# Kernel optimization log

Measured on AMD Instinct MI355X. Metric: run time of the kernel, lower is better.

## Reference

```python
import math
import jax, jax.numpy as jnp
import numpy as np

B, P, L = 32, 128, 64
DIN, TE, H, NH, NL = 16, 64, 512, 8, 2
DH = H // NH
DP = DIN + TE
TAU = 300.0
DELTA = 300.0

_PARAM_SPEC = [
    ("te_scale_w", (1, 1)), ("te_scale_b", (1,)),
    ("te_per_w", (TE - 1, 1)), ("te_per_b", (TE - 1,)),
    ("inp_w", (H, DP)), ("inp_b", (H,)),
    ("wq", (H, H)), ("bq", (H,)), ("wk", (H, H)), ("bk", (H,)),
    ("wv", (H, H)), ("bv", (H,)), ("wo", (H, H)), ("bo", (H,)),
    ("ffn_w1", (H, H)), ("ffn_b1", (H,)), ("ffn_w2", (H, H)), ("ffn_b2", (H,)),
    ("ln1_g", (H,)), ("ln1_b", (H,)), ("ln2_g", (H,)), ("ln2_b", (H,)),
    ("exists_bias", (1, 1, H)),
    ("gwq", (NL, H, H)), ("gbq", (NL, H)), ("gwk", (NL, H, H)), ("gbk", (NL, H)),
    ("gwv", (NL, H, H)), ("gbv", (NL, H)), ("gwo", (NL, H, H)), ("gbo", (NL, H)),
]


def setup_inputs() -> dict:
    key = jax.random.key(0)
    ks = jax.random.split(key, 3 + len(_PARAM_SPEC))
    inp = {
        "x": jax.random.normal(ks[0], (B, P, L, DIN), jnp.float32),
        "tt": jax.random.uniform(ks[1], (B, P, L, 1), jnp.float32),
        "mask": jax.random.randint(ks[2], (B, P, L, 1), 0, 2).astype(jnp.int32),
    }
    for i, (name, shp) in enumerate(_PARAM_SPEC):
        inp[name] = 0.02 * jax.random.normal(ks[3 + i], shp, jnp.float32)
    # LayerNorm affine params: gamma=1, beta=0
    inp["ln1_g"] = jnp.ones((H,), jnp.float32)
    inp["ln1_b"] = jnp.zeros((H,), jnp.float32)
    inp["ln2_g"] = jnp.ones((H,), jnp.float32)
    inp["ln2_b"] = jnp.zeros((H,), jnp.float32)
    return inp


def _layernorm(x, g, b, eps=1e-5):
    m = x.mean(-1, keepdims=True)
    v = ((x - m) ** 2).mean(-1, keepdims=True)
    return (x - m) / jnp.sqrt(v + eps) * g + b


def _time_bias(m):
    idx = jnp.arange(m)
    dist = jnp.abs(idx[:, None] - idx[None, :]).astype(jnp.float32) * DELTA
    return jnp.log(jnp.exp(-dist / TAU) + 1e-12)  # [P, P]


def _pos_encoding(p, d):
    pos = jnp.arange(p, dtype=jnp.float32)[:, None]
    div = jnp.exp(jnp.arange(0, d, 2, dtype=jnp.float32) * (-math.log(10000.0) / d))
    pe = jnp.zeros((p, d), jnp.float32)
    pe = pe.at[:, 0::2].set(jnp.sin(pos * div))
    pe = pe.at[:, 1::2].set(jnp.cos(pos * div))
    return pe


def reference(x, tt, mask,
              te_scale_w, te_scale_b, te_per_w, te_per_b,
              inp_w, inp_b, wq, bq, wk, bk, wv, bv, wo, bo,
              ffn_w1, ffn_b1, ffn_w2, ffn_b2, ln1_g, ln1_b, ln2_g, ln2_b,
              exists_bias, gwq, gbq, gwk, gbk, gwv, gbv, gwo, gbo):
    b, p, l, _ = x.shape
    # --- Learnable time embedding: scale linear + sin(periodic linear), concat ---
    te1 = tt @ te_scale_w.T + te_scale_b                      # [B,P,L,1]
    te2 = jnp.sin(tt @ te_per_w.T + te_per_b)                 # [B,P,L,TE-1]
    pts = jnp.concatenate([x, te1, te2], axis=-1)             # [B,P,L,DP]

    valid = (mask[..., 0] > 0).reshape(b * p, l)              # [N,L] bool
    h = (pts.reshape(b * p, l, DP) @ inp_w.T) + inp_b         # [N,L,H]

    has_any = jnp.any(valid, axis=1)                          # [N]
    key_pad = ~valid
    # Empty patches: unmask position 0 and zero its features
    key_pad = key_pad.at[:, 0].set(key_pad[:, 0] & has_any)
    pos0 = (jnp.arange(l) == 0)[None, :, None]
    h = jnp.where((~has_any)[:, None, None] & pos0, 0.0, h)

    # --- Intra-patch MHA (GAT) ---
    def heads(t, w, bias):
        return ((t @ w.T) + bias).reshape(b * p, l, NH, DH)
    q, k, v = heads(h, wq, bq), heads(h, wk, bk), heads(h, wv, bv)
    sc = jnp.einsum("nqhd,nkhd->nhqk", q, k) / math.sqrt(DH)
    sc = jnp.where(key_pad[:, None, None, :], -1e9, sc)
    z = jnp.einsum("nhqk,nkhd->nqhd", jax.nn.softmax(sc, axis=-1), v)
    z = z.reshape(b * p, l, H) @ wo.T + bo
    h = _layernorm(h + z, ln1_g, ln1_b)
    ffn = jax.nn.relu(h @ ffn_w1.T + ffn_b1) @ ffn_w2.T + ffn_b2
    h = _layernorm(h + ffn, ln2_g, ln2_b)

    # Masked mean pooling -> patch tokens
    w = valid.astype(jnp.float32)[..., None]                  # [N,L,1]
    denom = jnp.clip(w.sum(axis=1), 1.0)
    h = ((h * w).sum(axis=1) / denom).reshape(b, p, H)        # [B,P,H]

    # Exists bias for missing patches + positional encoding
    pexists = has_any.reshape(b, p).astype(jnp.float32)       # [B,P]
    h = h + exists_bias * (1.0 - pexists)[..., None]
    h = h + _pos_encoding(p, H)[None]

    # --- Patch-level time-biased graph attention stack (residual) ---
    tb = _time_bias(p)[None, None]                            # [1,1,P,P]
    kp = (pexists <= 0.0)[:, None, None, :]                   # [B,1,1,P]
    for li in range(NL):
        def gh(t, w, bias):
            return ((t @ w.T) + bias).reshape(b, p, NH, DH)
        q = gh(h, gwq[li], gbq[li])
        k = gh(h, gwk[li], gbk[li])
        v = gh(h, gwv[li], gbv[li])
        att = jnp.einsum("bqhd,bkhd->bhqk", q, k) / math.sqrt(DH) + tb
        att = jnp.where(kp, -1e9, att)
        out = jnp.einsum("bhqk,bkhd->bqhd", jax.nn.softmax(att, axis=-1), v)
        out = out.reshape(b, p, H) @ gwo[li].T + gbo[li]
        out = out * pexists[..., None]
        h = h + out
    return h
```

## Files before the change

kernel.cpp:

```cpp
#include <hip/hip_runtime.h>

#define NTOK 4096
#define CH   512
#define NCHUNK 8

typedef _Float16 f16;
typedef __attribute__((ext_vector_type(8))) _Float16 half8;
typedef __attribute__((ext_vector_type(4))) _Float16 half4;
typedef __attribute__((ext_vector_type(4))) float f32x4;

#define OFF_INPW 0
#define OFF_WQKV (512*128)
#define OFF_WO   (OFF_WQKV + 3*512*512)
#define OFF_W1   (OFF_WO + 512*512)
#define OFF_W2   (OFF_W1 + 512*512)
#define OFF_GW   (OFF_W2 + 512*512)
#define WBF_TOT  (OFF_GW + 8*512*512)

static __device__ __forceinline__ f32x4 mfma16(half8 a, half8 b, f32x4 c){
  return __builtin_amdgcn_mfma_f32_16x16x32_f16(a, b, c, 0, 0, 0);
}

static __device__ __forceinline__ void gld_lds16(const f16* g, f16* l){
  __builtin_amdgcn_global_load_lds(
      (const __attribute__((address_space(1))) void*)g,
      (__attribute__((address_space(3))) void*)l, 16, 0, 0);
}

#define FULL_BARRIER() do { \
    asm volatile("" ::: "memory"); \
    __builtin_amdgcn_s_barrier(); \
    __builtin_amdgcn_sched_barrier(0); \
  } while(0)

__global__ __launch_bounds__(256) void conv_weights(
    const float* __restrict__ inpw, const float* __restrict__ wq, const float* __restrict__ wk,
    const float* __restrict__ wv, const float* __restrict__ wo, const float* __restrict__ w1,
    const float* __restrict__ w2, const float* __restrict__ gwq, const float* __restrict__ gwk,
    const float* __restrict__ gwv, const float* __restrict__ gwo, f16* __restrict__ wbf,
    const float* __restrict__ bq, const float* __restrict__ bk, const float* __restrict__ bv,
    const float* __restrict__ gbq, const float* __restrict__ gbk, const float* __restrict__ gbv,
    float* __restrict__ biasb)
{
  int e = blockIdx.x*256 + threadIdx.x;
  int y = blockIdx.y;
  if (y == 0){
    if (e < 512*128){
      int row = e>>7, col = e&127;
      float v = (col < 80) ? inpw[row*80 + col] : 0.f;
      wbf[OFF_INPW + e] = (f16)v;
    }
    return;
  }
  if (y == 15){
    if (e < 1536){
      biasb[e] = (e < 512) ? bq[e] : (e < 1024 ? bk[e-512] : bv[e-1024]);
    } else if (e < 3*1536){
      int idx = e - 1536, li = idx/1536, c = idx - li*1536;
      float v = (c < 512) ? gbq[li*512 + c] : (c < 1024 ? gbk[li*512 + c-512] : gbv[li*512 + c-1024]);
      biasb[e] = v;
    }
    return;
  }
  if (e >= 512*512) return;
  const float* src; int off;
  if (y <= 6){
    const float* tab[6] = {wq, wk, wv, wo, w1, w2};
    src = tab[y-1]; off = OFF_WQKV + (y-1)*512*512;
  } else {
    int idx = y-7; int li = idx>>2, part = idx&3;
    const float* tab[4] = {gwq, gwk, gwv, gwo};
    src = tab[part] + (size_t)li*512*512; off = OFF_GW + idx*512*512;
  }
  wbf[off + e] = (f16)src[e];
}

__global__ __launch_bounds__(256) void build_mask(
    const int* __restrict__ mask, float* __restrict__ mb, float* __restrict__ pex)
{
  int wv = threadIdx.x>>6, lane = threadIdx.x&63;
  int n = blockIdx.x*4 + wv;
  int valid = mask[(size_t)n*64 + lane] > 0;
  unsigned long long ball = __ballot(valid);
  int hasany = (ball != 0ull);
  int masked = (lane == 0) ? (!valid && hasany) : (!valid);
  mb[(size_t)n*64 + lane] = masked ? -1e9f : 0.f;
  if (lane == 0) pex[n] = hasany ? 1.f : 0.f;
}

__global__ __launch_bounds__(256) void pts_build(
    const float* __restrict__ x, const float* __restrict__ tt,
    const float* __restrict__ tsw, const float* __restrict__ tsb,
    const float* __restrict__ tpw, const float* __restrict__ tpb,
    f16* __restrict__ pts, int rowbase)
{
  int e = blockIdx.x*256 + threadIdx.x;
  int r = e>>7, col = e&127;
  size_t grow = (size_t)rowbase + r;
  float v;
  if (col < 16) v = x[grow*16 + col];
  else if (col >= 80) v = 0.f;
  else {
    float t = tt[grow];
    if (col == 16) v = t*tsw[0] + tsb[0];
    else           v = __sinf(t*tpw[col-17] + tpb[col-17]);
  }
  pts[e] = (f16)v;
}

template<int RESID, bool RELU, bool OUTF32, bool ZEMPTY>
__global__ __launch_bounds__(256) void gemm128(
    const f16* __restrict__ A, const f16* __restrict__ W, const float* __restrict__ bias,
    void* __restrict__ Cout, const void* __restrict__ Rsd, const float* __restrict__ pex,
    int K, int lda, int ldc, int nbase, f16* __restrict__ dual)
{
  __shared__ __align__(16) f16 As[128][64];
  __shared__ __align__(16) f16 Bs[128][64];
  const int tid = threadIdx.x;
  const int m0 = blockIdx.x*128, n0 = blockIdx.y*128;
  const int wv = tid>>6, lane = tid&63, l15 = lane&15, quad = lane>>4;
  const int wm = (wv&1)*64, wn = (wv>>1)*64;
  const int srow = lane>>3;
  const int schunk = (lane&7) ^ srow;
  f32x4 acc[4][4] = {};
  for (int kc = 0; kc < K; kc += 64){
    __syncthreads();
    #pragma unroll
    for (int i=0; i<4; i++){
      const int rA = wv*32 + i*8;
      gld_lds16(A + (size_t)(m0 + rA + srow)*lda + kc + schunk*8, &As[rA][0]);
      gld_lds16(W + (size_t)(n0 + rA + srow)*K   + kc + schunk*8, &Bs[rA][0]);
    }
    __syncthreads();
    #pragma unroll
    for (int kk=0; kk<2; kk++){
      half8 av[4], bv8[4];
      #pragma unroll
      for (int t=0; t<4; t++){
        const int ra = wm + t*16 + l15;
        av[t]  = *(const half8*)(&As[ra][(((kk*4 + quad) ^ (ra&7)))*8]);
        const int rb = wn + t*16 + l15;
        bv8[t] = *(const half8*)(&Bs[rb][(((kk*4 + quad) ^ (rb&7)))*8]);
      }
      #pragma unroll
      for (int mt=0; mt<4; mt++)
        #pragma unroll
        for (int nt=0; nt<4; nt++)
          acc[mt][nt] = mfma16(av[mt], bv8[nt], acc[mt][nt]);
    }
  }
  #pragma unroll
  for (int mt=0; mt<4; mt++){
    #pragma unroll
    for (int nt=0; nt<4; nt++){
      #pragma unroll
      for (int i=0; i<4; i++){
        int gr = m0 + wm + mt*16 + quad*4 + i;
        int gc = n0 + wn + nt*16 + l15;
        float v = acc[mt][nt][i] + bias[gc];
        if (RELU) v = fmaxf(v, 0.f);
        if (RESID == 1) v += (float)((const f16*)Rsd)[(size_t)gr*ldc + gc];
        if (ZEMPTY){ if ((gr&63)==0 && pex[nbase + (gr>>6)]==0.f) v = 0.f; }
        if (RESID == 2) v = v*pex[gr] + ((const float*)Rsd)[(size_t)gr*ldc + gc];
        if (OUTF32) ((float*)Cout)[(size_t)gr*ldc + gc] = v;
        else        ((f16*)Cout)[(size_t)gr*ldc + gc] = (f16)v;
        if (RESID == 2){ if (dual) dual[(size_t)gr*ldc + gc] = (f16)v; }
      }
    }
  }
}

template<int RESID, bool RELU>
__global__ __launch_bounds__(512,2) void gemm256(
    const f16* __restrict__ A, const f16* __restrict__ W, const float* __restrict__ bias,
    f16* __restrict__ Cout, const f16* __restrict__ Rsd,
    int K, int lda, int ldc)
{
  __shared__ __align__(16) f16 As[2*2*128*64];
  __shared__ __align__(16) f16 Bs[2*2*128*64];

  const int tid = threadIdx.x;
  const int wv = tid>>6, lane = tid&63, l15 = lane&15, quad = lane>>4;
  const int wm = wv>>2;
  const int wn = wv&3;

  const int gx = gridDim.x, gy = gridDim.y;
  int nwg = gx*gy;
  int orig = blockIdx.x*gy + blockIdx.y;
  int qq = nwg>>3;
  int swz = (orig&7)*qq + (orig>>3);
  const int m0 = (swz/gy)*256, n0 = (swz%gy)*256;

  const int NT = K>>6;

  auto stage_half = [&](int t, int hf){
    int tc = t < NT ? t : NT-1;
    int kc = tc<<6;
    int b  = t & 1;
    #pragma unroll
    for (int i=0;i<2;i++){
      int idx = wv*2+i;
      int row = idx*8 + (lane>>3);
      int col = kc + (((lane&7) ^ (lane>>3))<<3);
      if (hf < 2)
        gld_lds16(A + (size_t)(m0 + hf*128 + row)*lda + col,
                  As + b*16384 + hf*8192 + idx*512);
      else
        gld_lds16(W + (size_t)(n0 + (hf-2)*128 + row)*K + col,
                  Bs + b*16384 + (hf-2)*8192 + idx*512);
    }
  };
  auto ldsA = [&](int b, int mt, int kk)->half8{
    int r = mt*16 + l15;
    int g = kk*4 + quad;
    return *(const half8*)(As + b*16384 + wm*8192 + r*64 + ((g ^ (r&7))<<3));
  };
  auto ldsB = [&](int b, int nt, int kk)->half8{
    int r = (wn&1)*64 + nt*16 + l15;
    int g = kk*4 + quad;
    return *(const half8*)(Bs + b*16384 + (wn>>1)*8192 + r*64 + ((g ^ (r&7))<<3));
  };

  half8 a[8], b0[4], b1[4];
  f32x4 acc[8][4] = {};
  auto mm8 = [&](int mb, half8* bq, int nb){
    __builtin_amdgcn_s_setprio(1);
    #pragma unroll
    for (int m=0;m<4;m++)
      #pragma unroll
      for (int n=0;n<2;n++)
        #pragma unroll
        for (int k=0;k<2;k++)
          acc[mb+m][nb+n] = mfma16(a[m*2+k], bq[n*2+k], acc[mb+m][nb+n]);
    __builtin_amdgcn_s_setprio(0);
  };

  stage_half(0,0); stage_half(0,1); stage_half(0,2); stage_half(0,3);
  stage_half(1,2); stage_half(1,3);
  asm volatile("s_waitcnt vmcnt(4)" ::: "memory");
  FULL_BARRIER();

  for (int t = 0; t < NT; t += 2){
    #pragma unroll
    for (int hv = 0; hv < 2; hv++){
      const int c  = t + hv;
      const int bf = hv;
      #pragma unroll
      for (int m=0;m<4;m++){ a[m*2]=ldsA(bf,m,0); a[m*2+1]=ldsA(bf,m,1); }
      #pragma unroll
      for (int n=0;n<2;n++){ b0[n*2]=ldsB(bf,n,0); b0[n*2+1]=ldsB(bf,n,1); }
      stage_half(c+1, 0);
      FULL_BARRIER();
      mm8(0, b0, 0);
      FULL_BARRIER();
      #pragma unroll
      for (int n=0;n<2;n++){ b1[n*2]=ldsB(bf,n+2,0); b1[n*2+1]=ldsB(bf,n+2,1); }
      stage_half(c+1, 1);
      FULL_BARRIER();
      mm8(0, b1, 2);
      FULL_BARRIER();
      #pragma unroll
      for (int m=0;m<4;m++){ a[m*2]=ldsA(bf,m+4,0); a[m*2+1]=ldsA(bf,m+4,1); }
      stage_half(c+2, 2);
      FULL_BARRIER();
      mm8(4, b1, 2);
      FULL_BARRIER();
      stage_half(c+2, 3);
      asm volatile("s_waitcnt vmcnt(4)" ::: "memory");
      FULL_BARRIER();
      mm8(4, b0, 0);
      FULL_BARRIER();
    }
  }

  #pragma unroll
  for (int mt=0; mt<8; mt++){
    #pragma unroll
    for (int nt=0; nt<4; nt++){
      #pragma unroll
      for (int i=0; i<4; i++){
        int gr = m0 + wm*128 + mt*16 + quad*4 + i;
        int gc = n0 + wn*64  + nt*16 + l15;
        float v = acc[mt][nt][i] + bias[gc];
        if (RELU) v = fmaxf(v, 0.f);
        if (RESID == 1) v += (float)Rsd[(size_t)gr*ldc + gc];
        __builtin_nontemporal_store((f16)v, &Cout[(size_t)gr*ldc + gc]);
      }
    }
  }
}

__global__ __launch_bounds__(128) void attn_patch(
    f16* __restrict__ qkv, const float* __restrict__ maskbias, int nbase)
{
  __shared__ f16 Vt[2][64][72];
  __shared__ f16 Ps[2][64][72];
  __shared__ float mbs[64];
  const int tid = threadIdx.x, wv = tid>>6, lane = tid&63, l15 = lane&15, quad = lane>>4;
  const int n = blockIdx.x, h = blockIdx.y*2 + wv;
  if (tid < 64) mbs[tid] = maskbias[(size_t)(nbase+n)*64 + tid];
  const f16* Vb = qkv + 1024 + h*64;
  for (int i=0; i<64; i++)
    Vt[wv][lane][i] = Vb[((size_t)n*64 + i)*1536 + lane];
  __syncthreads();
  const f16* Qb  = qkv + (size_t)n*64*1536 + h*64;
  const f16* Kbb = Qb + 512;
  f32x4 sacc[4][4] = {};
  #pragma unroll
  for (int kc=0; kc<2; kc++){
    half8 af[4], bf[4];
    #pragma unroll
    for (int t4=0; t4<4; t4++){
      af[t4] = *(const half8*)(Qb  + (size_t)(t4*16 + l15)*1536 + kc*32 + quad*8);
      bf[t4] = *(const half8*)(Kbb + (size_t)(t4*16 + l15)*1536 + kc*32 + quad*8);
    }
    #pragma unroll
    for (int ti=0; ti<4; ti++)
      #pragma unroll
      for (int tj=0; tj<4; tj++)
        sacc[ti][tj] = mfma16(af[ti], bf[tj], sacc[ti][tj]);
  }
  #pragma unroll
  for (int ti=0; ti<4; ti++){
    #pragma unroll
    for (int i=0; i<4; i++){
      float mx = -1e30f;
      #pragma unroll
      for (int tj=0; tj<4; tj++){
        float sv = sacc[ti][tj][i]*0.125f + mbs[tj*16 + l15];
        sacc[ti][tj][i] = sv;
        mx = fmaxf(mx, sv);
      }
      #pragma unroll
      for (int off=1; off<16; off<<=1) mx = fmaxf(mx, __shfl_xor(mx, off, 64));
      float sum = 0.f;
      #pragma unroll
      for (int tj=0; tj<4; tj++){
        float pv = __expf(sacc[ti][tj][i] - mx);
        sacc[ti][tj][i] = pv; sum += pv;
      }
      #pragma unroll
      for (int off=1; off<16; off<<=1) sum += __shfl_xor(sum, off, 64);
      float inv = 1.f/sum;
      int q = ti*16 + quad*4 + i;
      #pragma unroll
      for (int tj=0; tj<4; tj++)
        Ps[wv][q][tj*16 + l15] = (f16)(sacc[ti][tj][i]*inv);
    }
  }
  __syncthreads();
  f32x4 zacc[4][4] = {};
  #pragma unroll
  for (int kc=0; kc<2; kc++){
    half8 va[4], pb[4];
    #pragma unroll
    for (int t4=0; t4<4; t4++){
      va[t4] = *(const half8*)(&Vt[wv][t4*16 + l15][kc*32 + quad*8]);
      pb[t4] = *(const half8*)(&Ps[wv][t4*16 + l15][kc*32 + quad*8]);
    }
    #pragma unroll
    for (int ti2=0; ti2<4; ti2++)
      #pragma unroll
      for (int tj=0; tj<4; tj++)
        zacc[ti2][tj] = mfma16(va[ti2], pb[tj], zacc[ti2][tj]);
  }
  __syncthreads();
  #pragma unroll
  for (int ti2=0; ti2<4; ti2++)
    #pragma unroll
    for (int tj=0; tj<4; tj++){
      int q = tj*16 + l15, d0 = ti2*16 + quad*4;
      half4 pk;
      #pragma unroll
      for (int i=0; i<4; i++) pk[i] = (f16)zacc[ti2][tj][i];
      *(half4*)(&Vt[wv][q][d0]) = pk;
    }
  __syncthreads();
  #pragma unroll
  for (int i=0; i<8; i++){
    int q = i*8 + (lane>>3), d0 = (lane&7)*8;
    *(uint4*)(qkv + ((size_t)n*64 + q)*1536 + h*64 + d0) = *(const uint4*)(&Vt[wv][q][d0]);
  }
}

__global__ __launch_bounds__(256) void ln_rows(
    const f16* __restrict__ X, f16* __restrict__ Y,
    const float* __restrict__ g, const float* __restrict__ b)
{
  int wv = threadIdx.x>>6, lane = threadIdx.x&63;
  size_t row = (size_t)blockIdx.x*4 + wv;
  half8 raw = *(const half8*)(X + row*512 + lane*8);
  float xv[8];
  #pragma unroll
  for (int j=0; j<8; j++) xv[j] = (float)raw[j];
  float s = 0.f;
  #pragma unroll
  for (int j=0; j<8; j++) s += xv[j];
  #pragma unroll
  for (int off=1; off<64; off<<=1) s += __shfl_xor(s, off, 64);
  float mean = s*(1.f/512.f);
  float vs = 0.f;
  #pragma unroll
  for (int j=0; j<8; j++){ float d = xv[j]-mean; vs += d*d; }
  #pragma unroll
  for (int off=1; off<64; off<<=1) vs += __shfl_xor(vs, off, 64);
  float rstd = rsqrtf(vs*(1.f/512.f) + 1e-5f);
  half8 o;
  #pragma unroll
  for (int j=0; j<8; j++){
    int c = lane*8 + j;
    o[j] = (f16)((xv[j]-mean)*rstd*g[c] + b[c]);
  }
  *(half8*)(Y + row*512 + lane*8) = o;
}

__global__ __launch_bounds__(256) void pool_ln2(
    const f16* __restrict__ X, const int* __restrict__ mask,
    const float* __restrict__ g, const float* __restrict__ b, const float* __restrict__ eb,
    float* __restrict__ out, f16* __restrict__ hcopy, int nbase)
{
  __shared__ float mArr[64], rArr[64], vArr[64];
  const int tid = threadIdx.x, wv = tid>>6, lane = tid&63;
  const int n = blockIdx.x, ng = nbase + n, p = ng & 127;
  for (int j=0; j<16; j++){
    int l = wv*16 + j;
    half8 raw = *(const half8*)(X + ((size_t)n*64 + l)*512 + lane*8);
    float s=0.f, ss=0.f;
    #pragma unroll
    for (int jj=0; jj<8; jj++){ float f = (float)raw[jj]; s += f; ss += f*f; }
    #pragma unroll
    for (int off=1; off<64; off<<=1){ s += __shfl_xor(s, off, 64); ss += __shfl_xor(ss, off, 64); }
    if (lane == 0){
      float m = s*(1.f/512.f);
      mArr[l] = m; rArr[l] = rsqrtf(ss*(1.f/512.f) - m*m + 1e-5f);
    }
  }
  if (tid < 64) vArr[tid] = (mask[(size_t)ng*64 + tid] > 0) ? 1.f : 0.f;
  __syncthreads();
  float cnt = 0.f;
  #pragma unroll
  for (int l=0; l<64; l++) cnt += vArr[l];
  float denom = fmaxf(cnt, 1.f);
  float pexv = cnt > 0.f ? 1.f : 0.f;
  float a0=0.f, a1=0.f;
  for (int l=0; l<64; l++){
    float wgt = vArr[l], m = mArr[l], rs = rArr[l];
    float x0 = (float)X[((size_t)n*64+l)*512 + tid];
    float x1 = (float)X[((size_t)n*64+l)*512 + tid + 256];
    a0 += wgt*(x0-m)*rs; a1 += wgt*(x1-m)*rs;
  }
  #pragma unroll
  for (int k=0; k<2; k++){
    int c = tid + k*256;
    float acc = k ? a1 : a0;
    float fr = __expf(-(float)(c & ~1) * (9.210340371976184f/512.f));
    float ang = (float)p * fr;
    float pe = (c & 1) ? cosf(ang) : sinf(ang);
    float o = (g[c]*acc + b[c]*cnt)/denom + eb[c]*(1.f - pexv) + pe;
    out[(size_t)ng*512 + c] = o;
    hcopy[(size_t)ng*512 + c] = (f16)o;
  }
}

__global__ __launch_bounds__(256) void attn_graph(
    f16* __restrict__ qkv, const float* __restrict__ pexists)
{
  __shared__ f16 Vt[64][136];
  __shared__ f16 Ps[4][32][136];
  __shared__ float pxs[128];
  const int tid = threadIdx.x, wv = tid>>6, lane = tid&63, l15 = lane&15, quad = lane>>4;
  const int b = blockIdx.x, h = blockIdx.y;
  if (tid < 128) pxs[tid] = pexists[b*128 + tid];
  const f16* Vb = qkv + 1024 + h*64;
  for (int i=0; i<32; i++){
    int e = tid + i*256, k = e>>6, d = e&63;
    Vt[d][k] = Vb[((size_t)b*128 + k)*1536 + d];
  }
  __syncthreads();
  const f16* Qb = qkv + h*64;
  const f16* Kb = qkv + 512 + h*64;
  const int qb = wv*32;
  f32x4 sacc[2][8] = {};
  #pragma unroll
  for (int kc=0; kc<2; kc++){
    half8 af[2], bf[8];
    #pragma unroll
    for (int ti=0; ti<2; ti++)
      af[ti] = *(const half8*)(Qb + ((size_t)b*128 + qb + ti*16 + l15)*1536 + kc*32 + quad*8);
    #pragma unroll
    for (int tj=0; tj<8; tj++)
      bf[tj] = *(const half8*)(Kb + ((size_t)b*128 + tj*16 + l15)*1536 + kc*32 + quad*8);
    #pragma unroll
    for (int ti=0; ti<2; ti++)
      #pragma unroll
      for (int tj=0; tj<8; tj++)
        sacc[ti][tj] = mfma16(af[ti], bf[tj], sacc[ti][tj]);
  }
  #pragma unroll
  for (int ti=0; ti<2; ti++){
    #pragma unroll
    for (int i=0; i<4; i++){
      int q = qb + ti*16 + quad*4 + i;
      float mx = -1e30f;
      #pragma unroll
      for (int tj=0; tj<8; tj++){
        int col = tj*16 + l15;
        int dd = q - col; if (dd < 0) dd = -dd;
        float tb = __logf(__expf(-(float)dd) + 1e-12f);
        float sv = sacc[ti][tj][i]*0.125f + tb + (pxs[col] > 0.f ? 0.f : -1e9f);
        sacc[ti][tj][i] = sv;
        mx = fmaxf(mx, sv);
      }
      #pragma unroll
      for (int off=1; off<16; off<<=1) mx = fmaxf(mx, __shfl_xor(mx, off, 64));
      float sum = 0.f;
      #pragma unroll
      for (int tj=0; tj<8; tj++){
        float pv = __expf(sacc[ti][tj][i] - mx);
        sacc[ti][tj][i] = pv; sum += pv;
      }
      #pragma unroll
      for (int off=1; off<16; off<<=1) sum += __shfl_xor(sum, off, 64);
      float inv = 1.f/sum;
      int ql = ti*16 + quad*4 + i;
      #pragma unroll
      for (int tj=0; tj<8; tj++)
        Ps[wv][ql][tj*16 + l15] = (f16)(sacc[ti][tj][i]*inv);
    }
  }
  __syncthreads();
  f32x4 zacc[4][2] = {};
  #pragma unroll
  for (int kc=0; kc<4; kc++){
    half8 va[4], pb[2];
    #pragma unroll
    for (int ti2=0; ti2<4; ti2++)
      va[ti2] = *(const half8*)(&Vt[ti2*16 + l15][kc*32 + quad*8]);
    #pragma unroll
    for (int tjq=0; tjq<2; tjq++)
      pb[tjq] = *(const half8*)(&Ps[wv][tjq*16 + l15][kc*32 + quad*8]);
    #pragma unroll
    for (int ti2=0; ti2<4; ti2++)
      #pragma unroll
      for (int tjq=0; tjq<2; tjq++)
        zacc[ti2][tjq] = mfma16(va[ti2], pb[tjq], zacc[ti2][tjq]);
  }
  __syncthreads();
  #pragma unroll
  for (int ti2=0; ti2<4; ti2++)
    #pragma unroll
    for (int tjq=0; tjq<2; tjq++){
      int ql = tjq*16 + l15, d0 = ti2*16 + quad*4;
      half4 pk;
      #pragma unroll
      for (int i=0; i<4; i++) pk[i] = (f16)zacc[ti2][tjq][i];
      *(half4*)(&Ps[wv][ql][d0]) = pk;
    }
  __syncthreads();
  {
    int q = tid>>1, hf = tid&1;
    const f16* src = &Ps[q>>5][q&31][hf*32];
    #pragma unroll
    for (int j=0; j<4; j++)
      *(uint4*)(qkv + ((size_t)b*128 + q)*1536 + h*64 + hf*32 + j*8) = *(const uint4*)(src + j*8);
  }
}

extern "C" void kernel_launch(void* const* d_in, const int* in_sizes, int n_in,
                              void* d_out, int out_size, void* d_ws, size_t ws_size,
                              hipStream_t stream)
{
  (void)in_sizes; (void)n_in; (void)out_size; (void)ws_size;
  const float* x    = (const float*)d_in[0];
  const float* tt   = (const float*)d_in[1];
  const int*   mask = (const int*)  d_in[2];
  const float* tsw  = (const float*)d_in[3];
  const float* tsb  = (const float*)d_in[4];
  const float* tpw  = (const float*)d_in[5];
  const float* tpb  = (const float*)d_in[6];
  const float* inpw = (const float*)d_in[7];
  const float* inpb = (const float*)d_in[8];
  const float* wq   = (const float*)d_in[9];
  const float* bq   = (const float*)d_in[10];
  const float* wk   = (const float*)d_in[11];
  const float* bk   = (const float*)d_in[12];
  const float* wv   = (const float*)d_in[13];
  const float* bv   = (const float*)d_in[14];
  const float* wo   = (const float*)d_in[15];
  const float* bo   = (const float*)d_in[16];
  const float* w1   = (const float*)d_in[17];
  const float* b1   = (const float*)d_in[18];
  const float* w2   = (const float*)d_in[19];
  const float* b2   = (const float*)d_in[20];
  const float* ln1g = (const float*)d_in[21];
  const float* ln1b = (const float*)d_in[22];
  const float* ln2g = (const float*)d_in[23];
  const float* ln2b = (const float*)d_in[24];
  const float* eb   = (const float*)d_in[25];
  const float* gwq  = (const float*)d_in[26];
  const float* gbq  = (const float*)d_in[27];
  const float* gwk  = (const float*)d_in[28];
  const float* gbk  = (const float*)d_in[29];
  const float* gwv  = (const float*)d_in[30];
  const float* gbv  = (const float*)d_in[31];
  const float* gwo  = (const float*)d_in[32];
  const float* gbo  = (const float*)d_in[33];
  float* out = (float*)d_out;

  char* wp = (char*)d_ws;
  auto alloc = [&](size_t bytes)->char*{
    char* p = wp; wp += (bytes + 255) & ~(size_t)255; return p;
  };
  f16*   wbf   = (f16*)  alloc((size_t)WBF_TOT*2);
  float* mb    = (float*)alloc((size_t)NTOK*64*4);
  float* pex   = (float*)alloc((size_t)NTOK*4);
  float* biasb = (float*)alloc((size_t)3*1536*4);
  f16*   ptsb  = (f16*)  alloc((size_t)CH*64*128*2);
  f16*   bufA  = (f16*)  alloc((size_t)CH*64*512*2);
  f16*   bufB  = (f16*)  alloc((size_t)CH*64*512*2);
  f16*   bufC  = (f16*)  alloc((size_t)CH*64*512*2);
  f16*   qkv   = (f16*)  alloc((size_t)CH*64*1536*2);
  f16*   hbf   = (f16*)  alloc((size_t)NTOK*512*2);

  conv_weights<<<dim3(1024,16),256,0,stream>>>(inpw,wq,wk,wv,wo,w1,w2,gwq,gwk,gwv,gwo,wbf,
                                               bq,bk,bv,gbq,gbk,gbv,biasb);
  build_mask<<<NTOK/4,256,0,stream>>>(mask, mb, pex);

  const int MB  = CH*64/128;
  const int MB2 = CH*64/256;
  for (int ch=0; ch<NCHUNK; ch++){
    int nbase = ch*CH;
    int rowbase = nbase*64;
    pts_build<<<CH*64*128/256,256,0,stream>>>(x,tt,tsw,tsb,tpw,tpb,ptsb,rowbase);
    gemm128<0,false,false,true ><<<dim3(MB,4),256,0,stream>>>(ptsb, wbf+OFF_INPW, inpb, bufA, nullptr, pex, 128, 128, 512, nbase, nullptr);
    gemm256<0,false><<<dim3(MB2,6),512,0,stream>>>(bufA, wbf+OFF_WQKV, biasb, qkv, nullptr, 512, 512, 1536);
    attn_patch<<<dim3(CH,4),128,0,stream>>>(qkv, mb, nbase);
    gemm256<1,false><<<dim3(MB2,2),512,0,stream>>>(qkv, wbf+OFF_WO, bo, bufA, bufA, 512, 1536, 512);
    ln_rows<<<CH*64/4,256,0,stream>>>(bufA, bufB, ln1g, ln1b);
    gemm256<0,true ><<<dim3(MB2,2),512,0,stream>>>(bufB, wbf+OFF_W1, b1, bufC, nullptr, 512, 512, 512);
    gemm256<1,false><<<dim3(MB2,2),512,0,stream>>>(bufC, wbf+OFF_W2, b2, bufB, bufB, 512, 512, 512);
    pool_ln2<<<CH,256,0,stream>>>(bufB, mask, ln2g, ln2b, eb, out, hbf, nbase);
  }

  f16* qkvg = bufB;
  for (int li=0; li<2; li++){
    gemm128<0,false,false,false><<<dim3(32,12),256,0,stream>>>(hbf, wbf+OFF_GW + (size_t)li*4*512*512, biasb + 1536*(1+li), qkvg, nullptr, nullptr, 512, 512, 1536, 0, nullptr);
    attn_graph<<<dim3(32,8),256,0,stream>>>(qkvg, pex);
    gemm128<2,false,true ,false><<<dim3(32,4),256,0,stream>>>(qkvg, wbf+OFF_GW + (size_t)(li*4+3)*512*512, gbo+li*512, out, out, pex, 512, 1536, 512, 0, (li==0)? hbf : nullptr);
  }
}
```

Before: 2.614 ms.

## Triple-buffer A tiles with prefetch distance two in gemm256 main loop

```diff
diff --git a/kernel.cpp b/kernel.cpp
--- a/kernel.cpp
+++ b/kernel.cpp
@@ -176,7 +176,7 @@
     f16* __restrict__ Cout, const f16* __restrict__ Rsd,
     int K, int lda, int ldc)
 {
-  __shared__ __align__(16) f16 As[2*2*128*64];
+  __shared__ __align__(16) f16 As[3*2*128*64];
   __shared__ __align__(16) f16 Bs[2*2*128*64];
 
   const int tid = threadIdx.x;
@@ -184,8 +184,8 @@
   const int wm = wv>>2;
   const int wn = wv&3;
 
-  const int gx = gridDim.x, gy = gridDim.y;
-  int nwg = gx*gy;
+  const int gy = gridDim.y;
+  int nwg = gridDim.x*gy;
   int orig = blockIdx.x*gy + blockIdx.y;
   int qq = nwg>>3;
   int swz = (orig&7)*qq + (orig>>3);
@@ -193,32 +193,40 @@
 
   const int NT = K>>6;
 
-  auto stage_half = [&](int t, int hf){
+  auto stageA = [&](int t, int slot, int hf){
     int tc = t < NT ? t : NT-1;
     int kc = tc<<6;
-    int b  = t & 1;
     #pragma unroll
     for (int i=0;i<2;i++){
       int idx = wv*2+i;
       int row = idx*8 + (lane>>3);
       int col = kc + (((lane&7) ^ (lane>>3))<<3);
-      if (hf < 2)
-        gld_lds16(A + (size_t)(m0 + hf*128 + row)*lda + col,
-                  As + b*16384 + hf*8192 + idx*512);
-      else
-        gld_lds16(W + (size_t)(n0 + (hf-2)*128 + row)*K + col,
-                  Bs + b*16384 + (hf-2)*8192 + idx*512);
+      gld_lds16(A + (size_t)(m0 + hf*128 + row)*lda + col,
+                As + slot*16384 + hf*8192 + idx*512);
     }
   };
-  auto ldsA = [&](int b, int mt, int kk)->half8{
+  auto stageB = [&](int t, int hf){
+    int tc = t < NT ? t : NT-1;
+    int kc = tc<<6;
+    int slot = t & 1;
+    #pragma unroll
+    for (int i=0;i<2;i++){
+      int idx = wv*2+i;
+      int row = idx*8 + (lane>>3);
+      int col = kc + (((lane&7) ^ (lane>>3))<<3);
+      gld_lds16(W + (size_t)(n0 + hf*128 + row)*K + col,
+                Bs + slot*16384 + hf*8192 + idx*512);
+    }
+  };
+  auto ldsA = [&](int slot, int mt, int kk)->half8{
     int r = mt*16 + l15;
     int g = kk*4 + quad;
-    return *(const half8*)(As + b*16384 + wm*8192 + r*64 + ((g ^ (r&7))<<3));
+    return *(const half8*)(As + slot*16384 + wm*8192 + r*64 + ((g ^ (r&7))<<3));
   };
-  auto ldsB = [&](int b, int nt, int kk)->half8{
+  auto ldsB = [&](int slot, int nt, int kk)->half8{
     int r = (wn&1)*64 + nt*16 + l15;
     int g = kk*4 + quad;
-    return *(const half8*)(Bs + b*16384 + (wn>>1)*8192 + r*64 + ((g ^ (r&7))<<3));
+    return *(const half8*)(Bs + slot*16384 + (wn>>1)*8192 + r*64 + ((g ^ (r&7))<<3));
   };
 
   half8 a[8], b0[4], b1[4];
@@ -235,42 +243,42 @@
     __builtin_amdgcn_s_setprio(0);
   };
 
-  stage_half(0,0); stage_half(0,1); stage_half(0,2); stage_half(0,3);
-  stage_half(1,2); stage_half(1,3);
-  asm volatile("s_waitcnt vmcnt(4)" ::: "memory");
+  stageA(0,0,0); stageA(0,0,1); stageB(0,0); stageB(0,1);
+  stageA(1,1,0); stageA(1,1,1); stageB(1,0); stageB(1,1);
+  asm volatile("s_waitcnt vmcnt(8)" ::: "memory");
   FULL_BARRIER();
 
-  for (int t = 0; t < NT; t += 2){
-    #pragma unroll
-    for (int hv = 0; hv < 2; hv++){
-      const int c  = t + hv;
-      const int bf = hv;
-      #pragma unroll
-      for (int m=0;m<4;m++){ a[m*2]=ldsA(bf,m,0); a[m*2+1]=ldsA(bf,m,1); }
-      #pragma unroll
-      for (int n=0;n<2;n++){ b0[n*2]=ldsB(bf,n,0); b0[n*2+1]=ldsB(bf,n,1); }
-      stage_half(c+1, 0);
-      FULL_BARRIER();
-      mm8(0, b0, 0);
-      FULL_BARRIER();
-      #pragma unroll
-      for (int n=0;n<2;n++){ b1[n*2]=ldsB(bf,n+2,0); b1[n*2+1]=ldsB(bf,n+2,1); }
-      stage_half(c+1, 1);
-      FULL_BARRIER();
-      mm8(0, b1, 2);
-      FULL_BARRIER();
-      #pragma unroll
-      for (int m=0;m<4;m++){ a[m*2]=ldsA(bf,m+4,0); a[m*2+1]=ldsA(bf,m+4,1); }
-      stage_half(c+2, 2);
-      FULL_BARRIER();
-      mm8(4, b1, 2);
-      FULL_BARRIER();
-      stage_half(c+2, 3);
-      asm volatile("s_waitcnt vmcnt(4)" ::: "memory");
-      FULL_BARRIER();
-      mm8(4, b0, 0);
-      FULL_BARRIER();
-    }
+  int sc = 0;
+  #pragma unroll 1
+  for (int c = 0; c < NT; ++c){
+    const int bb = c & 1;
+    const int sn = (sc + 2 >= 3) ? sc - 1 : sc + 2;
+    #pragma unroll
+    for (int m=0;m<4;m++){ a[m*2]=ldsA(sc,m,0); a[m*2+1]=ldsA(sc,m,1); }
+    #pragma unroll
+    for (int n=0;n<2;n++){ b0[n*2]=ldsB(bb,n,0); b0[n*2+1]=ldsB(bb,n,1); }
+    FULL_BARRIER();
+    mm8(0, b0, 0);
+    FULL_BARRIER();
+    #pragma unroll
+    for (int n=0;n<2;n++){ b1[n*2]=ldsB(bb,n+2,0); b1[n*2+1]=ldsB(bb,n+2,1); }
+    FULL_BARRIER();
+    mm8(0, b1, 2);
+    FULL_BARRIER();
+    #pragma unroll
+    for (int m=0;m<4;m++){ a[m*2]=ldsA(sc,m+4,0); a[m*2+1]=ldsA(sc,m+4,1); }
+    stageA(c+2, sn, 0);
+    stageB(c+2, 0);
+    FULL_BARRIER();
+    mm8(4, b1, 2);
+    FULL_BARRIER();
+    stageA(c+2, sn, 1);
+    stageB(c+2, 1);
+    asm volatile("s_waitcnt vmcnt(8)" ::: "memory");
+    FULL_BARRIER();
+    mm8(4, b0, 0);
+    FULL_BARRIER();
+    sc = (sc + 1 >= 3) ? 0 : sc + 1;
   }
 
   #pragma unroll
@@ -284,7 +292,7 @@
         float v = acc[mt][nt][i] + bias[gc];
         if (RELU) v = fmaxf(v, 0.f);
         if (RESID == 1) v += (float)Rsd[(size_t)gr*ldc + gc];
-        __builtin_nontemporal_store((f16)v, &Cout[(size_t)gr*ldc + gc]);
+        Cout[(size_t)gr*ldc + gc] = (f16)v;
       }
     }
   }
```

Result: faster. 2.346 ms (-10.3%).
